# Kernel optimization log

Hardware: AMD Instinct MI355X
Metric: run time of the kernel (lower is better)

Reference implementation:

```python
import jax, jax.numpy as jnp
import numpy as np

HEADS = 8
NEG_SLOPE = 0.2  # PyG GATConv default LeakyReLU slope


def _gat_layer(x, src, dst, W, a_src, a_dst, bias, heads, out_ch):
    """PyG-style GATConv (concat heads, self-loops already appended, eval mode).
    x: [N, F_in]; src/dst: [E_tot] int; W: [F_in, heads*out_ch];
    a_src/a_dst: [heads, out_ch]; bias: [heads*out_ch].
    """
    N = x.shape[0]
    h = (x @ W).reshape(N, heads, out_ch)                      # [N, H, C]
    # per-node attention logits (gathered per edge as scalars, not features)
    al_s = jnp.einsum('nhc,hc->nh', h, a_src)                  # [N, H]
    al_d = jnp.einsum('nhc,hc->nh', h, a_dst)                  # [N, H]
    e = jax.nn.leaky_relu(al_s[src] + al_d[dst], negative_slope=NEG_SLOPE)  # [E, H]
    # segment softmax over incoming edges of each target node (stable)
    e_max = jax.ops.segment_max(e, dst, num_segments=N)        # self-loops => no empty segments
    ex = jnp.exp(e - e_max[dst])
    denom = jax.ops.segment_sum(ex, dst, num_segments=N)
    alpha = ex / (denom[dst] + 1e-16)                          # [E, H]
    # gather source features, weight, scatter-add to targets
    out = jax.ops.segment_sum(h[src] * alpha[:, :, None], dst, num_segments=N)  # [N, H, C]
    return out.reshape(N, heads * out_ch) + bias


def setup_inputs() -> dict:
    key = jax.random.key(0)
    ks = jax.random.split(key, 16)
    N, E, F_IN, NUM_CLASSES = 50000, 1600000, 128, 16
    s = 0.1
    return {
        'x': jax.random.normal(ks[0], (N, F_IN), dtype=jnp.float32),
        'edge_index': jax.random.randint(ks[1], (2, E), 0, N, dtype=jnp.int64),
        # GAT layer 1: 128 -> 8 heads x 8
        'W1': jax.random.normal(ks[2], (F_IN, 64), dtype=jnp.float32) * s,
        'a1_src': jax.random.normal(ks[3], (8, 8), dtype=jnp.float32) * s,
        'a1_dst': jax.random.normal(ks[4], (8, 8), dtype=jnp.float32) * s,
        'b1': jnp.zeros((64,), dtype=jnp.float32),
        # GAT layer 2: 64 -> 8 heads x 4
        'W2': jax.random.normal(ks[5], (64, 32), dtype=jnp.float32) * s,
        'a2_src': jax.random.normal(ks[6], (8, 4), dtype=jnp.float32) * s,
        'a2_dst': jax.random.normal(ks[7], (8, 4), dtype=jnp.float32) * s,
        'b2': jnp.zeros((32,), dtype=jnp.float32),
        # torch MultiheadAttention(32, 8): packed in_proj [96,32], out_proj [32,32]
        'in_proj_w': jax.random.normal(ks[8], (96, 32), dtype=jnp.float32) * s,
        'in_proj_b': jnp.zeros((96,), dtype=jnp.float32),
        'out_proj_w': jax.random.normal(ks[9], (32, 32), dtype=jnp.float32) * s,
        'out_proj_b': jnp.zeros((32,), dtype=jnp.float32),
        # fc: 32 -> num_classes
        'fc_w': jax.random.normal(ks[10], (NUM_CLASSES, 32), dtype=jnp.float32) * s,
        'fc_b': jnp.zeros((NUM_CLASSES,), dtype=jnp.float32),
    }


def reference(x, edge_index, W1, a1_src, a1_dst, b1, W2, a2_src, a2_dst, b2,
              in_proj_w, in_proj_b, out_proj_w, out_proj_b, fc_w, fc_b):
    N = x.shape[0]
    loops = jnp.arange(N, dtype=edge_index.dtype)
    src = jnp.concatenate([edge_index[0], loops])  # PyG add_self_loops=True
    dst = jnp.concatenate([edge_index[1], loops])

    h = jax.nn.elu(_gat_layer(x, src, dst, W1, a1_src, a1_dst, b1, HEADS, 8))   # [N, 64]
    h = jax.nn.elu(_gat_layer(h, src, dst, W2, a2_src, a2_dst, b2, HEADS, 4))   # [N, 32]

    # MultiheadAttention on h.unsqueeze(0): shape [1, N, 32] with torch's
    # seq-first layout => seq_len = 1, batch = N. Softmax over a single key
    # is identically 1 for every head, so out = out_proj(v_proj(h)).
    v = h @ in_proj_w[64:96].T + in_proj_b[64:96]   # v-projection slice of packed in_proj
    h = v @ out_proj_w.T + out_proj_b               # [N, 32]

    logits = h @ fc_w.T + fc_b                      # [N, num_classes]
    return jax.nn.log_softmax(logits, axis=1)
```

## Files before the change

kernel.cpp:

```cpp
#include <hip/hip_runtime.h>
#include <hip/hip_bf16.h>
#include <hip/hip_fp16.h>
#include <math.h>


#define BSHIFT 7
#define BMASK  ((1 << BSHIFT) - 1)
#define MAXNB  512
#define TILE   8192
#define XST    136
#define SMBYTES 36864
#define LESRC_MAX 6144

typedef __attribute__((ext_vector_type(8))) short short8;
typedef __attribute__((ext_vector_type(4))) float floatx4;
typedef __attribute__((ext_vector_type(2))) float floatx2;

__device__ __forceinline__ unsigned short f2bf(float f) {
    union { float f; unsigned int u; } v; v.f = f;
    unsigned int u = v.u;
    return (unsigned short)((u + 0x7FFFu + ((u >> 16) & 1u)) >> 16);
}
__device__ __forceinline__ float lrelu(float e) { return fmaxf(e, 0.2f * e); }
__device__ __forceinline__ float elu(float o) {
    return (o > 0.f) ? o : (__expf(o) - 1.f);
}

__global__ __launch_bounds__(256) void prep_kernel(
    const float* __restrict__ W, unsigned short* __restrict__ wtb,
    int* __restrict__ gcount) {
    int t = threadIdx.x;
    if (blockIdx.x == 0) { gcount[t] = 0; gcount[t + 256] = 0; }
    int idx = blockIdx.x * 256 + t;
    int n = idx >> 7, k = idx & 127;
    wtb[idx] = f2bf(W[k * 64 + n]);
}

__global__ __launch_bounds__(256) void fused_pre_kernel(
    const float* __restrict__ x, const unsigned short* __restrict__ wtb,
    const float* __restrict__ a_src, const float* __restrict__ a_dst,
    char* __restrict__ rec1, float* __restrict__ ald, int N, int GB,
    const int* __restrict__ ei, int E, int Et, int NB, int CAP,
    int* __restrict__ gcount, unsigned int* __restrict__ rec, int NT,
    const float* __restrict__ in_proj_w, const float* __restrict__ in_proj_b,
    const float* __restrict__ out_proj_w, const float* __restrict__ out_proj_b,
    const float* __restrict__ fc_w, const float* __restrict__ fc_b,
    float* __restrict__ M, float* __restrict__ bf) {
    __shared__ __align__(16) char sm[SMBYTES];
    int t = threadIdx.x;
    int bid = blockIdx.x;
    if (bid < GB) {
        unsigned short* xs = (unsigned short*)sm;
        unsigned short* wt = xs + 64 * XST;
        int nb = bid * 64;
#pragma unroll
        for (int r = 0; r < 8; ++r) {
            int p = t + 256 * r;
            int row = p >> 5;
            int c4  = p & 31;
            int n = nb + row;
            float4 v = (n < N) ? ((const float4*)x)[(size_t)n * 32 + c4]
                               : make_float4(0.f, 0.f, 0.f, 0.f);
            unsigned short* dst = &xs[row * XST + c4 * 4];
            dst[0] = f2bf(v.x); dst[1] = f2bf(v.y);
            dst[2] = f2bf(v.z); dst[3] = f2bf(v.w);
        }
        {
            int n = t & 63, kg = t >> 6;
#pragma unroll
            for (int c = 0; c < 4; ++c) {
                int k0 = kg * 32 + c * 8;
                *(short8*)&wt[n * XST + k0] = *(const short8*)&wtb[n * 128 + k0];
            }
        }
        __syncthreads();
        int wave = t >> 6, lane = t & 63;
        int m16 = lane & 15, quad = lane >> 4;
        floatx4 acc[4];
#pragma unroll
        for (int i = 0; i < 4; ++i) acc[i] = (floatx4){0.f, 0.f, 0.f, 0.f};
#pragma unroll
        for (int k = 0; k < 4; ++k) {
            int koff = k * 32 + quad * 8;
            short8 afrag = *(const short8*)&xs[(wave * 16 + m16) * XST + koff];
#pragma unroll
            for (int nt = 0; nt < 4; ++nt) {
                short8 bfrag = *(const short8*)&wt[(nt * 16 + m16) * XST + koff];
                acc[nt] = __builtin_amdgcn_mfma_f32_16x16x32_bf16(afrag, bfrag, acc[nt], 0, 0, 0);
            }
        }
        __syncthreads();
        float* hs = (float*)sm;
#pragma unroll
        for (int nt = 0; nt < 4; ++nt)
#pragma unroll
            for (int r = 0; r < 4; ++r)
                hs[(wave * 16 + quad * 4 + r) * 65 + nt * 16 + m16] = acc[nt][r];
        __syncthreads();
        float asv = a_src[lane], adv = a_dst[lane];
        for (int itn = 0; itn < 16; ++itn) {
            int nl = wave * 16 + itn;
            int n = nb + nl;
            if (n >= N) break;
            float v = hs[nl * 65 + lane];
            float ps = v * asv, pd = v * adv;
            ps += __shfl_xor(ps, 1); ps += __shfl_xor(ps, 2); ps += __shfl_xor(ps, 4);
            pd += __shfl_xor(pd, 1); pd += __shfl_xor(pd, 2); pd += __shfl_xor(pd, 4);
            float av = __shfl(ps, (lane & 7) * 8);
            if ((lane & 7) == 0)
                ald[n * 8 + (lane >> 3)] = pd;
            if (lane < 8) {
                const float* hr = &hs[nl * 65 + lane * 8];
                int pk0 = __builtin_amdgcn_cvt_pk_fp8_f32(hr[0], hr[1], 0, false);
                pk0 = __builtin_amdgcn_cvt_pk_fp8_f32(hr[2], hr[3], pk0, true);
                int pk1 = __builtin_amdgcn_cvt_pk_fp8_f32(hr[4], hr[5], 0, false);
                pk1 = __builtin_amdgcn_cvt_pk_fp8_f32(hr[6], hr[7], pk1, true);
                *(__half*)(rec1 + (size_t)n * 80 + 2 * lane) = __float2half(av);
                uint2 w2v;
                w2v.x = (unsigned)pk0;
                w2v.y = (unsigned)pk1;
                *(uint2*)(rec1 + (size_t)n * 80 + 16 + 8 * lane) = w2v;
            }
        }
    } else if (bid < GB + NT) {
        unsigned int* lrec = (unsigned int*)sm;
        int* h   = (int*)(sm + TILE * 4);
        int* cur = (int*)(sm + TILE * 4 + MAXNB * 4);
        for (int i = t; i < NB; i += 256) h[i] = 0;
        int tile0 = (bid - GB) * TILE;
        int cnt = Et - tile0; if (cnt > TILE) cnt = TILE;
        __syncthreads();
        for (int j = t; j < cnt; j += 256) {
            int jj = tile0 + j;
            int srcv, d;
            if (jj < E) { srcv = ei[jj]; d = ei[E + jj]; } else { srcv = jj - E; d = jj - E; }
            lrec[j] = (unsigned)srcv | ((unsigned)d << 16);
            atomicAdd(&h[d >> BSHIFT], 1);
        }
        __syncthreads();
        for (int i = t; i < NB; i += 256)
            cur[i] = h[i] ? atomicAdd(&gcount[i], h[i]) : 0;
        __syncthreads();
        for (int j = t; j < cnt; j += 256) {
            unsigned v = lrec[j];
            int b = v >> (16 + BSHIFT);
            int pos = atomicAdd(&cur[b], 1);
            if (pos < CAP)
                rec[(size_t)b * CAP + pos] =
                    (v & 0xFFFFu) | ((((v >> 16) & BMASK)) << 16);
        }
    } else {
        float* Wvo = (float*)sm;
        float* bvo = (float*)(sm + 4096);
        const float* Wv = in_proj_w + 64 * 32;
        const float* bv = in_proj_b + 64;
        for (int idx = t; idx < 1024; idx += 256) {
            int i = idx >> 5, j = idx & 31;
            float acc = 0.f;
            for (int k = 0; k < 32; ++k) acc += out_proj_w[i * 32 + k] * Wv[k * 32 + j];
            Wvo[idx] = acc;
        }
        if (t < 32) {
            float acc = 0.f;
            for (int k = 0; k < 32; ++k) acc += out_proj_w[t * 32 + k] * bv[k];
            bvo[t] = acc + out_proj_b[t];
        }
        __syncthreads();
        for (int idx = t; idx < 16 * 32; idx += 256) {
            int cc = idx >> 5, j = idx & 31;
            float acc = 0.f;
            for (int i = 0; i < 32; ++i) acc += fc_w[cc * 32 + i] * Wvo[i * 32 + j];
            M[idx] = acc;
        }
        if (t < 16) {
            float acc = 0.f;
            for (int i = 0; i < 32; ++i) acc += fc_w[t * 32 + i] * bvo[i];
            bf[t] = acc + fc_b[t];
        }
    }
}

__global__ __launch_bounds__(256) void csr_finalize_kernel(
    const unsigned int* __restrict__ rec, const int* __restrict__ gcount,
    int* __restrict__ rowp, unsigned short* __restrict__ esrc,
    int N, int Et, int CAP) {
    __shared__ int h[128];
    __shared__ int nb[128];
    __shared__ int cur[128];
    __shared__ int ssum[256];
    __shared__ unsigned short lesrc[LESRC_MAX];
    int b = blockIdx.x, t = threadIdx.x;
    size_t rbase = (size_t)b * CAP;
    int cnt = gcount[b]; if (cnt > CAP) cnt = CAP;
    if (t < 128) h[t] = 0;
    int acc = 0;
    for (int i = t; i < b; i += 256) {
        int v = gcount[i];
        acc += (v < CAP) ? v : CAP;
    }
    ssum[t] = acc;
    __syncthreads();
    for (int off = 128; off >= 1; off >>= 1) {
        if (t < off) ssum[t] += ssum[t + off];
        __syncthreads();
    }
    int obase = ssum[0];
    for (int i = t; i < cnt; i += 256)
        atomicAdd(&h[(rec[rbase + i] >> 16) & 127], 1);
    __syncthreads();
    if (t == 0) {
        int run = 0;
        for (int i = 0; i < 128; ++i) { nb[i] = run; run += h[i]; }
    }
    __syncthreads();
    if (t < 128) cur[t] = nb[t];
    int n0 = b << BSHIFT;
    if (t < 128 && n0 + t < N) rowp[n0 + t] = obase + nb[t];
    if (b == 0 && t == 0) rowp[N] = Et;
    __syncthreads();
    for (int i = t; i < cnt; i += 256) {
        unsigned r = rec[rbase + i];
        int pos = atomicAdd(&cur[(r >> 16) & 127], 1);
        lesrc[pos] = (unsigned short)(r & 0xFFFFu);
    }
    __syncthreads();
    for (int i = t; i < cnt; i += 256)
        esrc[obase + i] = lesrc[i];
}

__global__ __launch_bounds__(256) void gat_agg64_g2_kernel(
    const int* __restrict__ rowp, const unsigned short* __restrict__ esrc,
    const char* __restrict__ rec1, const float* __restrict__ ald_arr,
    const float* __restrict__ bias,
    const float* __restrict__ W2, const float* __restrict__ a2s,
    const float* __restrict__ a2d,
    char* __restrict__ rec2, float* __restrict__ ald2, int N) {
    __shared__ __align__(16) float W2p[2][8][32][4];
    __shared__ __align__(16) float oL[4][64];
    __shared__ __align__(16) float h2L[4][32];
    int t = threadIdx.x;
    const int lane = t & 63;
    const int wv = t >> 6;
    const int e = lane >> 3;
    const int c = lane & 7;
    const int aoff = 2 * c;
    const int foff = 16 + 8 * c;
    int n = blockIdx.x * 4 + wv;
    bool active = n < N;
    if (active) {
        float aldv = ald_arr[n * 8 + c];
        int beg = rowp[n], end = rowp[n + 1];
        int deg = end - beg;
        float dA = 0.f, dB = 0.f;
        floatx2 A0 = {0.f, 0.f}, A1 = {0.f, 0.f}, A2 = {0.f, 0.f}, A3 = {0.f, 0.f};
        floatx2 B0 = {0.f, 0.f}, B1 = {0.f, 0.f}, B2 = {0.f, 0.f}, B3 = {0.f, 0.f};
        if (deg <= 48) {
            int s[6];
#pragma unroll
            for (int g = 0; g < 6; ++g) {
                int p = beg + g * 8 + e;
                s[g] = esrc[(p < end) ? p : beg];
            }
            float ev[6];
            uint2 gg[6];
#pragma unroll
            for (int g = 0; g < 6; ++g) {
                const char* r = rec1 + (size_t)s[g] * 80;
                ev[g] = __half2float(*(const __half*)(r + aoff));
                gg[g] = *(const uint2*)(r + foff);
            }
#pragma unroll
            for (int g = 0; g < 6; ++g) {
                bool vv = (beg + g * 8 + e) < end;
                float w = vv ? __expf(lrelu(ev[g] + aldv)) : 0.f;
                if ((g & 1) == 0) {
                    dA += w;
                    A0 += w * __builtin_amdgcn_cvt_pk_f32_fp8(gg[g].x, false);
                    A1 += w * __builtin_amdgcn_cvt_pk_f32_fp8(gg[g].x, true);
                    A2 += w * __builtin_amdgcn_cvt_pk_f32_fp8(gg[g].y, false);
                    A3 += w * __builtin_amdgcn_cvt_pk_f32_fp8(gg[g].y, true);
                } else {
                    dB += w;
                    B0 += w * __builtin_amdgcn_cvt_pk_f32_fp8(gg[g].x, false);
                    B1 += w * __builtin_amdgcn_cvt_pk_f32_fp8(gg[g].x, true);
                    B2 += w * __builtin_amdgcn_cvt_pk_f32_fp8(gg[g].y, false);
                    B3 += w * __builtin_amdgcn_cvt_pk_f32_fp8(gg[g].y, true);
                }
            }
        } else {
            int i = beg;
            for (; i + 32 <= end; i += 32) {
                int s0 = esrc[i + e],      s1 = esrc[i + 8 + e];
                int s2 = esrc[i + 16 + e], s3 = esrc[i + 24 + e];
                const char* r0 = rec1 + (size_t)s0 * 80;
                const char* r1 = rec1 + (size_t)s1 * 80;
                const char* r2 = rec1 + (size_t)s2 * 80;
                const char* r3 = rec1 + (size_t)s3 * 80;
                float e0 = __half2float(*(const __half*)(r0 + aoff));
                float e1 = __half2float(*(const __half*)(r1 + aoff));
                float e2 = __half2float(*(const __half*)(r2 + aoff));
                float e3 = __half2float(*(const __half*)(r3 + aoff));
                uint2 g0 = *(const uint2*)(r0 + foff);
                uint2 g1 = *(const uint2*)(r1 + foff);
                uint2 g2 = *(const uint2*)(r2 + foff);
                uint2 g3 = *(const uint2*)(r3 + foff);
                float w0 = __expf(lrelu(e0 + aldv));
                float w1 = __expf(lrelu(e1 + aldv));
                float w2 = __expf(lrelu(e2 + aldv));
                float w3 = __expf(lrelu(e3 + aldv));
                dA += w0 + w2; dB += w1 + w3;
                A0 += w0 * __builtin_amdgcn_cvt_pk_f32_fp8(g0.x, false);
                A1 += w0 * __builtin_amdgcn_cvt_pk_f32_fp8(g0.x, true);
                A2 += w0 * __builtin_amdgcn_cvt_pk_f32_fp8(g0.y, false);
                A3 += w0 * __builtin_amdgcn_cvt_pk_f32_fp8(g0.y, true);
                B0 += w1 * __builtin_amdgcn_cvt_pk_f32_fp8(g1.x, false);
                B1 += w1 * __builtin_amdgcn_cvt_pk_f32_fp8(g1.x, true);
                B2 += w1 * __builtin_amdgcn_cvt_pk_f32_fp8(g1.y, false);
                B3 += w1 * __builtin_amdgcn_cvt_pk_f32_fp8(g1.y, true);
                A0 += w2 * __builtin_amdgcn_cvt_pk_f32_fp8(g2.x, false);
                A1 += w2 * __builtin_amdgcn_cvt_pk_f32_fp8(g2.x, true);
                A2 += w2 * __builtin_amdgcn_cvt_pk_f32_fp8(g2.y, false);
                A3 += w2 * __builtin_amdgcn_cvt_pk_f32_fp8(g2.y, true);
                B0 += w3 * __builtin_amdgcn_cvt_pk_f32_fp8(g3.x, false);
                B1 += w3 * __builtin_amdgcn_cvt_pk_f32_fp8(g3.x, true);
                B2 += w3 * __builtin_amdgcn_cvt_pk_f32_fp8(g3.y, false);
                B3 += w3 * __builtin_amdgcn_cvt_pk_f32_fp8(g3.y, true);
            }
            for (; i < end; i += 32) {
                int i0 = i + e, i1 = i + 8 + e, i2 = i + 16 + e, i3 = i + 24 + e;
                bool v0 = i0 < end, v1 = i1 < end, v2 = i2 < end, v3 = i3 < end;
                int c0 = v0 ? i0 : beg;
                int c1 = v1 ? i1 : beg;
                int c2 = v2 ? i2 : beg;
                int c3 = v3 ? i3 : beg;
                int s0 = esrc[c0], s1 = esrc[c1], s2 = esrc[c2], s3 = esrc[c3];
                const char* r0 = rec1 + (size_t)s0 * 80;
                const char* r1 = rec1 + (size_t)s1 * 80;
                const char* r2 = rec1 + (size_t)s2 * 80;
                const char* r3 = rec1 + (size_t)s3 * 80;
                float e0 = __half2float(*(const __half*)(r0 + aoff));
                float e1 = __half2float(*(const __half*)(r1 + aoff));
                float e2 = __half2float(*(const __half*)(r2 + aoff));
                float e3 = __half2float(*(const __half*)(r3 + aoff));
                uint2 g0 = *(const uint2*)(r0 + foff);
                uint2 g1 = *(const uint2*)(r1 + foff);
                uint2 g2 = *(const uint2*)(r2 + foff);
                uint2 g3 = *(const uint2*)(r3 + foff);
                float w0 = v0 ? __expf(lrelu(e0 + aldv)) : 0.f;
                float w1 = v1 ? __expf(lrelu(e1 + aldv)) : 0.f;
                float w2 = v2 ? __expf(lrelu(e2 + aldv)) : 0.f;
                float w3 = v3 ? __expf(lrelu(e3 + aldv)) : 0.f;
                dA += w0 + w2; dB += w1 + w3;
                A0 += w0 * __builtin_amdgcn_cvt_pk_f32_fp8(g0.x, false);
                A1 += w0 * __builtin_amdgcn_cvt_pk_f32_fp8(g0.x, true);
                A2 += w0 * __builtin_amdgcn_cvt_pk_f32_fp8(g0.y, false);
                A3 += w0 * __builtin_amdgcn_cvt_pk_f32_fp8(g0.y, true);
                B0 += w1 * __builtin_amdgcn_cvt_pk_f32_fp8(g1.x, false);
                B1 += w1 * __builtin_amdgcn_cvt_pk_f32_fp8(g1.x, true);
                B2 += w1 * __builtin_amdgcn_cvt_pk_f32_fp8(g1.y, false);
                B3 += w1 * __builtin_amdgcn_cvt_pk_f32_fp8(g1.y, true);
                A0 += w2 * __builtin_amdgcn_cvt_pk_f32_fp8(g2.x, false);
                A1 += w2 * __builtin_amdgcn_cvt_pk_f32_fp8(g2.x, true);
                A2 += w2 * __builtin_amdgcn_cvt_pk_f32_fp8(g2.y, false);
                A3 += w2 * __builtin_amdgcn_cvt_pk_f32_fp8(g2.y, true);
                B0 += w3 * __builtin_amdgcn_cvt_pk_f32_fp8(g3.x, false);
                B1 += w3 * __builtin_amdgcn_cvt_pk_f32_fp8(g3.x, true);
                B2 += w3 * __builtin_amdgcn_cvt_pk_f32_fp8(g3.y, false);
                B3 += w3 * __builtin_amdgcn_cvt_pk_f32_fp8(g3.y, true);
            }
        }
        float d = dA + dB;
        float P0 = A0.x + B0.x, P1 = A0.y + B0.y;
        float P2 = A1.x + B1.x, P3 = A1.y + B1.y;
        float P4 = A2.x + B2.x, P5 = A2.y + B2.y;
        float P6 = A3.x + B3.x, P7 = A3.y + B3.y;
        d  += __shfl_xor(d, 8);  d  += __shfl_xor(d, 16);  d  += __shfl_xor(d, 32);
        P0 += __shfl_xor(P0, 8); P0 += __shfl_xor(P0, 16); P0 += __shfl_xor(P0, 32);
        P1 += __shfl_xor(P1, 8); P1 += __shfl_xor(P1, 16); P1 += __shfl_xor(P1, 32);
        P2 += __shfl_xor(P2, 8); P2 += __shfl_xor(P2, 16); P2 += __shfl_xor(P2, 32);
        P3 += __shfl_xor(P3, 8); P3 += __shfl_xor(P3, 16); P3 += __shfl_xor(P3, 32);
        P4 += __shfl_xor(P4, 8); P4 += __shfl_xor(P4, 16); P4 += __shfl_xor(P4, 32);
        P5 += __shfl_xor(P5, 8); P5 += __shfl_xor(P5, 16); P5 += __shfl_xor(P5, 32);
        P6 += __shfl_xor(P6, 8); P6 += __shfl_xor(P6, 16); P6 += __shfl_xor(P6, 32);
        P7 += __shfl_xor(P7, 8); P7 += __shfl_xor(P7, 16); P7 += __shfl_xor(P7, 32);
        float inv = 1.f / (d + 1e-16f);
        float4 bv0 = ((const float4*)bias)[2 * c];
        float4 bv1 = ((const float4*)bias)[2 * c + 1];
        float o0 = elu(P0 * inv + bv0.x);
        float o1 = elu(P1 * inv + bv0.y);
        float o2 = elu(P2 * inv + bv0.z);
        float o3 = elu(P3 * inv + bv0.w);
        float o4 = elu(P4 * inv + bv1.x);
        float o5 = elu(P5 * inv + bv1.y);
        float o6 = elu(P6 * inv + bv1.z);
        float o7 = elu(P7 * inv + bv1.w);
        if (lane < 8) {
            *(float4*)&oL[wv][c * 8]     = make_float4(o0, o1, o2, o3);
            *(float4*)&oL[wv][c * 8 + 4] = make_float4(o4, o5, o6, o7);
        }
    }
    for (int idx = t; idx < 2048; idx += 256) {
        int k = idx >> 5, l = idx & 31;
        W2p[k >> 5][(k & 31) >> 2][l][k & 3] = W2[idx];
    }
    __syncthreads();
    if (!active) return;
    const int l = lane & 31, kh = lane >> 5;
    const float* orow = &oL[wv][kh * 32];
    float a0 = 0.f, a1 = 0.f, a2 = 0.f, a3 = 0.f;
#pragma unroll
    for (int g = 0; g < 8; ++g) {
        float4 ov = *(const float4*)&orow[g * 4];
        float4 wv4 = *(const float4*)&W2p[kh][g][l][0];
        a0 += ov.x * wv4.x; a1 += ov.y * wv4.y;
        a2 += ov.z * wv4.z; a3 += ov.w * wv4.w;
    }
    float acc = (a0 + a1) + (a2 + a3);
    acc += __shfl_xor(acc, 32);
    float ps = acc * a2s[l], pd = acc * a2d[l];
    ps += __shfl_xor(ps, 1); ps += __shfl_xor(ps, 2);
    pd += __shfl_xor(pd, 1); pd += __shfl_xor(pd, 2);
    float psv = __shfl(ps, (lane & 7) * 4);
    if (lane < 32) {
        h2L[wv][l] = acc;
        if ((l & 3) == 0) ald2[n * 8 + (l >> 2)] = pd;
    }
    if (lane < 8) {
        const float* hr = &h2L[wv][lane * 4];
        int pk = __builtin_amdgcn_cvt_pk_fp8_f32(hr[0], hr[1], 0, false);
        pk = __builtin_amdgcn_cvt_pk_fp8_f32(hr[2], hr[3], pk, true);
        *(__half*)(rec2 + (size_t)n * 48 + 2 * lane) = __float2half(psv);
        *(unsigned*)(rec2 + (size_t)n * 48 + 16 + 4 * lane) = (unsigned)pk;
    }
}

__global__ __launch_bounds__(256) void gat_agg32_fin_kernel(
    const int* __restrict__ rowp, const unsigned short* __restrict__ esrc,
    const char* __restrict__ rec2, const float* __restrict__ ald_arr,
    const float* __restrict__ bias,
    const float* __restrict__ M, const float* __restrict__ bf,
    float* __restrict__ out, int N) {
    __shared__ __align__(16) float Mp[8][16][4];
    __shared__ float bfs[16];
    __shared__ __align__(16) float oL[4][32];
    int t = threadIdx.x;
    const int lane = t & 63;
    const int wv = t >> 6;
    const int e = lane >> 3;
    const int c = lane & 7;
    const int aoff = 2 * c;
    const int foff = 16 + 4 * c;
    int n = blockIdx.x * 4 + wv;
    bool active = n < N;
    if (active) {
        float aldv = ald_arr[n * 8 + c];
        int beg = rowp[n], end = rowp[n + 1];
        int deg = end - beg;
        float d0 = 0.f, d1 = 0.f, d2 = 0.f, d3 = 0.f;
        floatx2 p0a = {0.f, 0.f}, p0b = {0.f, 0.f};
        floatx2 p1a = {0.f, 0.f}, p1b = {0.f, 0.f};
        floatx2 p2a = {0.f, 0.f}, p2b = {0.f, 0.f};
        floatx2 p3a = {0.f, 0.f}, p3b = {0.f, 0.f};
        if (deg <= 64) {
            int s[8];
#pragma unroll
            for (int g = 0; g < 8; ++g) {
                int p = beg + g * 8 + e;
                s[g] = esrc[(p < end) ? p : beg];
            }
            float ev[8];
            unsigned gg[8];
#pragma unroll
            for (int g = 0; g < 8; ++g) {
                const char* r = rec2 + (size_t)s[g] * 48;
                ev[g] = __half2float(*(const __half*)(r + aoff));
                gg[g] = *(const unsigned*)(r + foff);
            }
#pragma unroll
            for (int g = 0; g < 8; ++g) {
                bool vv = (beg + g * 8 + e) < end;
                float w = vv ? __expf(lrelu(ev[g] + aldv)) : 0.f;
                if ((g & 3) == 0) {
                    d0 += w;
                    p0a += w * __builtin_amdgcn_cvt_pk_f32_fp8(gg[g], false);
                    p0b += w * __builtin_amdgcn_cvt_pk_f32_fp8(gg[g], true);
                } else if ((g & 3) == 1) {
                    d1 += w;
                    p1a += w * __builtin_amdgcn_cvt_pk_f32_fp8(gg[g], false);
                    p1b += w * __builtin_amdgcn_cvt_pk_f32_fp8(gg[g], true);
                } else if ((g & 3) == 2) {
                    d2 += w;
                    p2a += w * __builtin_amdgcn_cvt_pk_f32_fp8(gg[g], false);
                    p2b += w * __builtin_amdgcn_cvt_pk_f32_fp8(gg[g], true);
                } else {
                    d3 += w;
                    p3a += w * __builtin_amdgcn_cvt_pk_f32_fp8(gg[g], false);
                    p3b += w * __builtin_amdgcn_cvt_pk_f32_fp8(gg[g], true);
                }
            }
        } else {
            int base = beg;
            for (; base + 32 <= end; base += 32) {
                int s0 = esrc[base + e],      s1 = esrc[base + 8 + e];
                int s2 = esrc[base + 16 + e], s3 = esrc[base + 24 + e];
                const char* r0 = rec2 + (size_t)s0 * 48;
                const char* r1 = rec2 + (size_t)s1 * 48;
                const char* r2 = rec2 + (size_t)s2 * 48;
                const char* r3 = rec2 + (size_t)s3 * 48;
                float e0 = __half2float(*(const __half*)(r0 + aoff)) + aldv;
                float e1 = __half2float(*(const __half*)(r1 + aoff)) + aldv;
                float e2 = __half2float(*(const __half*)(r2 + aoff)) + aldv;
                float e3 = __half2float(*(const __half*)(r3 + aoff)) + aldv;
                unsigned g0 = *(const unsigned*)(r0 + foff);
                unsigned g1 = *(const unsigned*)(r1 + foff);
                unsigned g2 = *(const unsigned*)(r2 + foff);
                unsigned g3 = *(const unsigned*)(r3 + foff);
                float w0 = __expf(lrelu(e0));
                float w1 = __expf(lrelu(e1));
                float w2 = __expf(lrelu(e2));
                float w3 = __expf(lrelu(e3));
                d0 += w0; d1 += w1; d2 += w2; d3 += w3;
                p0a += w0 * __builtin_amdgcn_cvt_pk_f32_fp8(g0, false);
                p0b += w0 * __builtin_amdgcn_cvt_pk_f32_fp8(g0, true);
                p1a += w1 * __builtin_amdgcn_cvt_pk_f32_fp8(g1, false);
                p1b += w1 * __builtin_amdgcn_cvt_pk_f32_fp8(g1, true);
                p2a += w2 * __builtin_amdgcn_cvt_pk_f32_fp8(g2, false);
                p2b += w2 * __builtin_amdgcn_cvt_pk_f32_fp8(g2, true);
                p3a += w3 * __builtin_amdgcn_cvt_pk_f32_fp8(g3, false);
                p3b += w3 * __builtin_amdgcn_cvt_pk_f32_fp8(g3, true);
            }
            for (; base < end; base += 32) {
                int i0 = base + e;
                int i1 = base + 8 + e;
                int i2 = base + 16 + e;
                int i3 = base + 24 + e;
                bool v0 = i0 < end, v1 = i1 < end, v2 = i2 < end, v3 = i3 < end;
                int c0 = v0 ? i0 : beg;
                int c1 = v1 ? i1 : beg;
                int c2 = v2 ? i2 : beg;
                int c3 = v3 ? i3 : beg;
                int s0 = esrc[c0], s1 = esrc[c1], s2 = esrc[c2], s3 = esrc[c3];
                const char* r0 = rec2 + (size_t)s0 * 48;
                const char* r1 = rec2 + (size_t)s1 * 48;
                const char* r2 = rec2 + (size_t)s2 * 48;
                const char* r3 = rec2 + (size_t)s3 * 48;
                float e0 = __half2float(*(const __half*)(r0 + aoff)) + aldv;
                float e1 = __half2float(*(const __half*)(r1 + aoff)) + aldv;
                float e2 = __half2float(*(const __half*)(r2 + aoff)) + aldv;
                float e3 = __half2float(*(const __half*)(r3 + aoff)) + aldv;
                unsigned g0 = *(const unsigned*)(r0 + foff);
                unsigned g1 = *(const unsigned*)(r1 + foff);
                unsigned g2 = *(const unsigned*)(r2 + foff);
                unsigned g3 = *(const unsigned*)(r3 + foff);
                float w0 = v0 ? __expf(lrelu(e0)) : 0.f;
                float w1 = v1 ? __expf(lrelu(e1)) : 0.f;
                float w2 = v2 ? __expf(lrelu(e2)) : 0.f;
                float w3 = v3 ? __expf(lrelu(e3)) : 0.f;
                d0 += w0; d1 += w1; d2 += w2; d3 += w3;
                p0a += w0 * __builtin_amdgcn_cvt_pk_f32_fp8(g0, false);
                p0b += w0 * __builtin_amdgcn_cvt_pk_f32_fp8(g0, true);
                p1a += w1 * __builtin_amdgcn_cvt_pk_f32_fp8(g1, false);
                p1b += w1 * __builtin_amdgcn_cvt_pk_f32_fp8(g1, true);
                p2a += w2 * __builtin_amdgcn_cvt_pk_f32_fp8(g2, false);
                p2b += w2 * __builtin_amdgcn_cvt_pk_f32_fp8(g2, true);
                p3a += w3 * __builtin_amdgcn_cvt_pk_f32_fp8(g3, false);
                p3b += w3 * __builtin_amdgcn_cvt_pk_f32_fp8(g3, true);
            }
        }
        float d = (d0 + d1) + (d2 + d3);
        floatx2 Pa = (p0a + p1a) + (p2a + p3a);
        floatx2 Pb = (p0b + p1b) + (p2b + p3b);
        float P0 = Pa.x, P1 = Pa.y, P2 = Pb.x, P3 = Pb.y;
        d  += __shfl_xor(d, 8);  d  += __shfl_xor(d, 16);  d  += __shfl_xor(d, 32);
        P0 += __shfl_xor(P0, 8); P0 += __shfl_xor(P0, 16); P0 += __shfl_xor(P0, 32);
        P1 += __shfl_xor(P1, 8); P1 += __shfl_xor(P1, 16); P1 += __shfl_xor(P1, 32);
        P2 += __shfl_xor(P2, 8); P2 += __shfl_xor(P2, 16); P2 += __shfl_xor(P2, 32);
        P3 += __shfl_xor(P3, 8); P3 += __shfl_xor(P3, 16); P3 += __shfl_xor(P3, 32);
        float inv = 1.f / (d + 1e-16f);
        float4 bv = ((const float4*)bias)[c];
        float o0 = elu(P0 * inv + bv.x);
        float o1 = elu(P1 * inv + bv.y);
        float o2 = elu(P2 * inv + bv.z);
        float o3 = elu(P3 * inv + bv.w);
        if (lane < 8) *(float4*)&oL[wv][c * 4] = make_float4(o0, o1, o2, o3);
    }
    for (int i = t; i < 512; i += 256) {
        int j = i >> 5, k = i & 31;
        Mp[k >> 2][j][k & 3] = M[i];
    }
    if (t < 16) bfs[t] = bf[t];
    __syncthreads();
    if (!active) return;
    const int j = lane & 15;
    const float* orow = oL[wv];
    float a0 = 0.f, a1 = 0.f, a2 = 0.f, a3 = 0.f;
#pragma unroll
    for (int g = 0; g < 8; ++g) {
        float4 ov = *(const float4*)&orow[g * 4];
        float4 mv = *(const float4*)&Mp[g][j][0];
        a0 += ov.x * mv.x; a1 += ov.y * mv.y;
        a2 += ov.z * mv.z; a3 += ov.w * mv.w;
    }
    float logit = (a0 + a1) + (a2 + a3) + bfs[j];
    float mx = logit;
    mx = fmaxf(mx, __shfl_xor(mx, 1));
    mx = fmaxf(mx, __shfl_xor(mx, 2));
    mx = fmaxf(mx, __shfl_xor(mx, 4));
    mx = fmaxf(mx, __shfl_xor(mx, 8));
    float ex = __expf(logit - mx);
    float se = ex;
    se += __shfl_xor(se, 1);
    se += __shfl_xor(se, 2);
    se += __shfl_xor(se, 4);
    se += __shfl_xor(se, 8);
    float res = logit - (mx + __logf(se));
    if (lane < 16) out[(size_t)n * 16 + j] = res;
}

extern "C" void kernel_launch(void* const* d_in, const int* in_sizes, int n_in,
                              void* d_out, int out_size, void* d_ws, size_t ws_size,
                              hipStream_t stream) {
    const float* x   = (const float*)d_in[0];
    const int*   ei  = (const int*)d_in[1];
    const float* W1  = (const float*)d_in[2];
    const float* a1s = (const float*)d_in[3];
    const float* a1d = (const float*)d_in[4];
    const float* b1  = (const float*)d_in[5];
    const float* W2  = (const float*)d_in[6];
    const float* a2s = (const float*)d_in[7];
    const float* a2d = (const float*)d_in[8];
    const float* b2  = (const float*)d_in[9];
    const float* ipw = (const float*)d_in[10];
    const float* ipb = (const float*)d_in[11];
    const float* opw = (const float*)d_in[12];
    const float* opb = (const float*)d_in[13];
    const float* fcw = (const float*)d_in[14];
    const float* fcb = (const float*)d_in[15];
    float* out = (float*)d_out;

    int N = in_sizes[0] / 128;
    int E = in_sizes[1] / 2;
    int Et = E + N;
    int NB = (N + BMASK) >> BSHIFT;
    int NTILES = (Et + TILE - 1) / TILE;
    int GB = (N + 63) / 64;
    int CAP = Et / NB;
    CAP = CAP + CAP / 8 + 256;
    CAP = (CAP + 255) & ~255;
    if (CAP > LESRC_MAX) CAP = LESRC_MAX;

    char* ws = (char*)d_ws;
    size_t off = 0;
    auto alloc = [&](size_t bytes) -> void* {
        void* p = ws + off;
        off += bytes;
        off = (off + 255) & ~(size_t)255;
        return p;
    };
    int*   bcount = (int*)alloc(MAXNB * 4);
    unsigned int*   rec  = (unsigned int*)alloc((size_t)NB * CAP * 4);
    int*   rowp   = (int*)alloc((size_t)(N + 1) * 4);
    unsigned short* esrc = (unsigned short*)alloc((size_t)Et * 2);
    char* rec1   = (char*)alloc((size_t)N * 80);
    float* al1d  = (float*)alloc((size_t)N * 8 * 4);
    char* rec2   = (char*)alloc((size_t)N * 48);
    float* al2d  = (float*)alloc((size_t)N * 8 * 4);
    float* Mf    = (float*)alloc(512 * 4);
    float* bff   = (float*)alloc(16 * 4);
    unsigned short* wtb = (unsigned short*)alloc(64 * 128 * 2);
    (void)ws_size; (void)n_in; (void)out_size;

    prep_kernel<<<32, 256, 0, stream>>>(W1, wtb, bcount);
    fused_pre_kernel<<<GB + NTILES + 1, 256, 0, stream>>>(
        x, wtb, a1s, a1d, rec1, al1d, N, GB,
        ei, E, Et, NB, CAP, bcount, rec, NTILES,
        ipw, ipb, opw, opb, fcw, fcb, Mf, bff);
    csr_finalize_kernel<<<NB, 256, 0, stream>>>(rec, bcount, rowp, esrc, N, Et, CAP);

    gat_agg64_g2_kernel<<<(N + 3) / 4, 256, 0, stream>>>(
        rowp, esrc, rec1, al1d, b1, W2, a2s, a2d, rec2, al2d, N);
    gat_agg32_fin_kernel<<<(N + 3) / 4, 256, 0, stream>>>(
        rowp, esrc, rec2, al2d, b2, Mf, bff, out, N);
}
```

Measured before the change: 207.1 us.

## Replace bucketed CSR build with fixed-capacity per-node adjacency slots

Drops the two-pass bucketed CSR construction (per-tile histogram, global bucket reservation and the csr_finalize kernel). In its place each edge does a global atomicAdd on its destination's counter and writes its source into a fixed 128-slot row per node. The W1 bf16 transpose also moves into the GEMM blocks, so prep_kernel is removed and a memset zeros the counters. This saves a kernel launch and a full pass over the edges, but adds a heavily contended global atomic per edge and a padded adjacency layout. Any edges past 128 for a node are silently dropped.

```diff
diff --git a/kernel.cpp b/kernel.cpp
--- a/kernel.cpp
+++ b/kernel.cpp
@@ -4,13 +4,10 @@
 #include <math.h>
 
 
-#define BSHIFT 7
-#define BMASK  ((1 << BSHIFT) - 1)
-#define MAXNB  512
 #define TILE   8192
 #define XST    136
 #define SMBYTES 36864
-#define LESRC_MAX 6144
+#define CAPN   128
 
 typedef __attribute__((ext_vector_type(8))) short short8;
 typedef __attribute__((ext_vector_type(4))) float floatx4;
@@ -26,22 +23,12 @@
     return (o > 0.f) ? o : (__expf(o) - 1.f);
 }
 
-__global__ __launch_bounds__(256) void prep_kernel(
-    const float* __restrict__ W, unsigned short* __restrict__ wtb,
-    int* __restrict__ gcount) {
-    int t = threadIdx.x;
-    if (blockIdx.x == 0) { gcount[t] = 0; gcount[t + 256] = 0; }
-    int idx = blockIdx.x * 256 + t;
-    int n = idx >> 7, k = idx & 127;
-    wtb[idx] = f2bf(W[k * 64 + n]);
-}
-
 __global__ __launch_bounds__(256) void fused_pre_kernel(
-    const float* __restrict__ x, const unsigned short* __restrict__ wtb,
+    const float* __restrict__ x, const float* __restrict__ W,
     const float* __restrict__ a_src, const float* __restrict__ a_dst,
     char* __restrict__ rec1, float* __restrict__ ald, int N, int GB,
-    const int* __restrict__ ei, int E, int Et, int NB, int CAP,
-    int* __restrict__ gcount, unsigned int* __restrict__ rec, int NT,
+    const int* __restrict__ ei, int E, int Et,
+    int* __restrict__ cnt, unsigned short* __restrict__ esrc2, int NT,
     const float* __restrict__ in_proj_w, const float* __restrict__ in_proj_b,
     const float* __restrict__ out_proj_w, const float* __restrict__ out_proj_b,
     const float* __restrict__ fc_w, const float* __restrict__ fc_b,
@@ -66,11 +53,14 @@
             dst[2] = f2bf(v.z); dst[3] = f2bf(v.w);
         }
         {
-            int n = t & 63, kg = t >> 6;
+            int nn = t & 63, kg = t >> 6;
 #pragma unroll
             for (int c = 0; c < 4; ++c) {
                 int k0 = kg * 32 + c * 8;
-                *(short8*)&wt[n * XST + k0] = *(const short8*)&wtb[n * 128 + k0];
+                unsigned short* dst = &wt[nn * XST + k0];
+#pragma unroll
+                for (int j = 0; j < 8; ++j)
+                    dst[j] = f2bf(W[(k0 + j) * 64 + nn]);
             }
         }
         __syncthreads();
@@ -123,31 +113,14 @@
             }
         }
     } else if (bid < GB + NT) {
-        unsigned int* lrec = (unsigned int*)sm;
-        int* h   = (int*)(sm + TILE * 4);
-        int* cur = (int*)(sm + TILE * 4 + MAXNB * 4);
-        for (int i = t; i < NB; i += 256) h[i] = 0;
         int tile0 = (bid - GB) * TILE;
-        int cnt = Et - tile0; if (cnt > TILE) cnt = TILE;
-        __syncthreads();
-        for (int j = t; j < cnt; j += 256) {
-            int jj = tile0 + j;
+        int jend = tile0 + TILE; if (jend > Et) jend = Et;
+        for (int j = tile0 + t; j < jend; j += 256) {
             int srcv, d;
-            if (jj < E) { srcv = ei[jj]; d = ei[E + jj]; } else { srcv = jj - E; d = jj - E; }
-            lrec[j] = (unsigned)srcv | ((unsigned)d << 16);
-            atomicAdd(&h[d >> BSHIFT], 1);
-        }
-        __syncthreads();
-        for (int i = t; i < NB; i += 256)
-            cur[i] = h[i] ? atomicAdd(&gcount[i], h[i]) : 0;
-        __syncthreads();
-        for (int j = t; j < cnt; j += 256) {
-            unsigned v = lrec[j];
-            int b = v >> (16 + BSHIFT);
-            int pos = atomicAdd(&cur[b], 1);
-            if (pos < CAP)
-                rec[(size_t)b * CAP + pos] =
-                    (v & 0xFFFFu) | ((((v >> 16) & BMASK)) << 16);
+            if (j < E) { srcv = ei[j]; d = ei[E + j]; } else { srcv = j - E; d = j - E; }
+            int pos = atomicAdd(&cnt[d], 1);
+            if (pos < CAPN)
+                esrc2[(size_t)d * CAPN + pos] = (unsigned short)srcv;
         }
     } else {
         float* Wvo = (float*)sm;
@@ -180,56 +153,8 @@
     }
 }
 
-__global__ __launch_bounds__(256) void csr_finalize_kernel(
-    const unsigned int* __restrict__ rec, const int* __restrict__ gcount,
-    int* __restrict__ rowp, unsigned short* __restrict__ esrc,
-    int N, int Et, int CAP) {
-    __shared__ int h[128];
-    __shared__ int nb[128];
-    __shared__ int cur[128];
-    __shared__ int ssum[256];
-    __shared__ unsigned short lesrc[LESRC_MAX];
-    int b = blockIdx.x, t = threadIdx.x;
-    size_t rbase = (size_t)b * CAP;
-    int cnt = gcount[b]; if (cnt > CAP) cnt = CAP;
-    if (t < 128) h[t] = 0;
-    int acc = 0;
-    for (int i = t; i < b; i += 256) {
-        int v = gcount[i];
-        acc += (v < CAP) ? v : CAP;
-    }
-    ssum[t] = acc;
-    __syncthreads();
-    for (int off = 128; off >= 1; off >>= 1) {
-        if (t < off) ssum[t] += ssum[t + off];
-        __syncthreads();
-    }
-    int obase = ssum[0];
-    for (int i = t; i < cnt; i += 256)
-        atomicAdd(&h[(rec[rbase + i] >> 16) & 127], 1);
-    __syncthreads();
-    if (t == 0) {
-        int run = 0;
-        for (int i = 0; i < 128; ++i) { nb[i] = run; run += h[i]; }
-    }
-    __syncthreads();
-    if (t < 128) cur[t] = nb[t];
-    int n0 = b << BSHIFT;
-    if (t < 128 && n0 + t < N) rowp[n0 + t] = obase + nb[t];
-    if (b == 0 && t == 0) rowp[N] = Et;
-    __syncthreads();
-    for (int i = t; i < cnt; i += 256) {
-        unsigned r = rec[rbase + i];
-        int pos = atomicAdd(&cur[(r >> 16) & 127], 1);
-        lesrc[pos] = (unsigned short)(r & 0xFFFFu);
-    }
-    __syncthreads();
-    for (int i = t; i < cnt; i += 256)
-        esrc[obase + i] = lesrc[i];
-}
-
 __global__ __launch_bounds__(256) void gat_agg64_g2_kernel(
-    const int* __restrict__ rowp, const unsigned short* __restrict__ esrc,
+    const int* __restrict__ cnt, const unsigned short* __restrict__ esrc,
     const char* __restrict__ rec1, const float* __restrict__ ald_arr,
     const float* __restrict__ bias,
     const float* __restrict__ W2, const float* __restrict__ a2s,
@@ -249,8 +174,9 @@
     bool active = n < N;
     if (active) {
         float aldv = ald_arr[n * 8 + c];
-        int beg = rowp[n], end = rowp[n + 1];
-        int deg = end - beg;
+        int deg = cnt[n]; if (deg > CAPN) deg = CAPN;
+        int beg = n * CAPN;
+        int end = beg + deg;
         float dA = 0.f, dB = 0.f;
         floatx2 A0 = {0.f, 0.f}, A1 = {0.f, 0.f}, A2 = {0.f, 0.f}, A3 = {0.f, 0.f};
         floatx2 B0 = {0.f, 0.f}, B1 = {0.f, 0.f}, B2 = {0.f, 0.f}, B3 = {0.f, 0.f};
@@ -435,7 +361,7 @@
 }
 
 __global__ __launch_bounds__(256) void gat_agg32_fin_kernel(
-    const int* __restrict__ rowp, const unsigned short* __restrict__ esrc,
+    const int* __restrict__ cnt, const unsigned short* __restrict__ esrc,
     const char* __restrict__ rec2, const float* __restrict__ ald_arr,
     const float* __restrict__ bias,
     const float* __restrict__ M, const float* __restrict__ bf,
@@ -454,8 +380,9 @@
     bool active = n < N;
     if (active) {
         float aldv = ald_arr[n * 8 + c];
-        int beg = rowp[n], end = rowp[n + 1];
-        int deg = end - beg;
+        int deg = cnt[n]; if (deg > CAPN) deg = CAPN;
+        int beg = n * CAPN;
+        int end = beg + deg;
         float d0 = 0.f, d1 = 0.f, d2 = 0.f, d3 = 0.f;
         floatx2 p0a = {0.f, 0.f}, p0b = {0.f, 0.f};
         floatx2 p1a = {0.f, 0.f}, p1b = {0.f, 0.f};
@@ -641,13 +568,8 @@
     int N = in_sizes[0] / 128;
     int E = in_sizes[1] / 2;
     int Et = E + N;
-    int NB = (N + BMASK) >> BSHIFT;
     int NTILES = (Et + TILE - 1) / TILE;
     int GB = (N + 63) / 64;
-    int CAP = Et / NB;
-    CAP = CAP + CAP / 8 + 256;
-    CAP = (CAP + 255) & ~255;
-    if (CAP > LESRC_MAX) CAP = LESRC_MAX;
 
     char* ws = (char*)d_ws;
     size_t off = 0;
@@ -657,28 +579,23 @@
         off = (off + 255) & ~(size_t)255;
         return p;
     };
-    int*   bcount = (int*)alloc(MAXNB * 4);
-    unsigned int*   rec  = (unsigned int*)alloc((size_t)NB * CAP * 4);
-    int*   rowp   = (int*)alloc((size_t)(N + 1) * 4);
-    unsigned short* esrc = (unsigned short*)alloc((size_t)Et * 2);
+    int* cnt = (int*)alloc((size_t)N * 4);
+    unsigned short* esrc2 = (unsigned short*)alloc((size_t)N * CAPN * 2);
     char* rec1   = (char*)alloc((size_t)N * 80);
     float* al1d  = (float*)alloc((size_t)N * 8 * 4);
     char* rec2   = (char*)alloc((size_t)N * 48);
     float* al2d  = (float*)alloc((size_t)N * 8 * 4);
     float* Mf    = (float*)alloc(512 * 4);
     float* bff   = (float*)alloc(16 * 4);
-    unsigned short* wtb = (unsigned short*)alloc(64 * 128 * 2);
     (void)ws_size; (void)n_in; (void)out_size;
 
-    prep_kernel<<<32, 256, 0, stream>>>(W1, wtb, bcount);
+    hipMemsetAsync(cnt, 0, (size_t)N * 4, stream);
     fused_pre_kernel<<<GB + NTILES + 1, 256, 0, stream>>>(
-        x, wtb, a1s, a1d, rec1, al1d, N, GB,
-        ei, E, Et, NB, CAP, bcount, rec, NTILES,
+        x, W1, a1s, a1d, rec1, al1d, N, GB,
+        ei, E, Et, cnt, esrc2, NTILES,
         ipw, ipb, opw, opb, fcw, fcb, Mf, bff);
-    csr_finalize_kernel<<<NB, 256, 0, stream>>>(rec, bcount, rowp, esrc, N, Et, CAP);
-
     gat_agg64_g2_kernel<<<(N + 3) / 4, 256, 0, stream>>>(
-        rowp, esrc, rec1, al1d, b1, W2, a2s, a2d, rec2, al2d, N);
+        cnt, esrc2, rec1, al1d, b1, W2, a2s, a2d, rec2, al2d, N);
     gat_agg32_fin_kernel<<<(N + 3) / 4, 256, 0, stream>>>(
-        rowp, esrc, rec2, al2d, b2, Mf, bff, out, N);
+        cnt, esrc2, rec2, al2d, b2, Mf, bff, out, N);
 }
```

After: 250.7 us. 21.1% more time.
